# Kernel tuning notes

Hardware: AMD Instinct MI355X
Metric: run time of the kernel (lower is better)

## Reference

```python
import jax, jax.numpy as jnp
import numpy as np
import math

DIM = 1024
H = 16
D = 64
M = 64  # num_features
B = 1
N = 2048


def _orf_omega(key):
    # Orthogonal Random Features: stack Q^T blocks from QR of Gaussian [D,D]
    blocks = []
    n_blocks = (M + D - 1) // D
    for i in range(n_blocks):
        G = jax.random.normal(jax.random.fold_in(key, i), (D, D), dtype=jnp.float32)
        Q, _ = jnp.linalg.qr(G)
        blocks.append(Q.T)
    return jnp.concatenate(blocks, axis=0)[:M]  # [M, D]


def setup_inputs() -> dict:
    key = jax.random.key(0)
    ks = jax.random.split(key, 7)
    inner = H * D
    x = jax.random.normal(ks[0], (B, N, DIM), dtype=jnp.float32)
    omega = _orf_omega(ks[1])
    wq = jax.random.normal(ks[2], (inner, DIM), dtype=jnp.float32) * 0.02
    wk = jax.random.normal(ks[3], (inner, DIM), dtype=jnp.float32) * 0.02
    wv = jax.random.normal(ks[4], (inner, DIM), dtype=jnp.float32) * 0.02
    wo = jax.random.normal(ks[5], (DIM, inner), dtype=jnp.float32) * 0.02
    bo = jnp.zeros((DIM,), dtype=jnp.float32)
    return {"x": x, "omega": omega, "wq": wq, "wk": wk, "wv": wv, "wo": wo, "bo": bo}


def _phi(x, omega):
    # x: [B,H,N,D], omega: [M,D] -> [B,H,N,M]
    proj = jnp.einsum('bhnd,md->bhnm', x, omega)
    norm = 0.5 * jnp.sum(x * x, axis=-1, keepdims=True)
    return jnp.exp(proj - norm) / math.sqrt(M)


def _heads(t):
    b, n, _ = t.shape
    return t.reshape(b, n, H, D).transpose(0, 2, 1, 3)  # [B,H,N,D]


def reference(x, omega, wq, wk, wv, wo, bo):
    b, n, _ = x.shape
    q = _heads(x @ wq.T)
    k = _heads(x @ wk.T)
    v = _heads(x @ wv.T)
    phi_q = _phi(q, omega)  # [B,H,N,M]
    phi_k = _phi(k, omega)
    # causal linear attention: cumulative KV state (naive materialization, faithful to source)
    kv = jnp.einsum('bhnm,bhnd->bhnmd', phi_k, v)       # [B,H,N,M,D]
    kv_cumsum = jnp.cumsum(kv, axis=2)
    k_cumsum = jnp.cumsum(phi_k, axis=2)                # [B,H,N,M]
    out = jnp.einsum('bhnm,bhnmd->bhnd', phi_q, kv_cumsum)
    z = 1.0 / (jnp.einsum('bhnm,bhnm->bhn', phi_q, k_cumsum) + 1e-6)
    out = out * z[..., None]
    out = out.transpose(0, 2, 1, 3).reshape(b, n, H * D)
    return out @ wo.T + bo
```

## Files before the change

kernel.cpp:

```cpp
#include <hip/hip_runtime.h>
#include <hip/hip_bf16.h>

typedef __hip_bfloat16 bf16;
typedef __attribute__((ext_vector_type(8))) short bf16x8;
typedef __attribute__((ext_vector_type(8))) _Float16 f16x8;
typedef __attribute__((ext_vector_type(4))) float f32x4;

constexpr int N_TOK = 2048;
constexpr int DIMM  = 1024;
constexpr int NH    = 16;
constexpr int HD    = 64;
constexpr int FM    = 64;
constexpr int NC    = 32;
constexpr int CS    = 64;

__device__ __forceinline__ float b2f(bf16 v) { return __bfloat162float(v); }
__device__ __forceinline__ unsigned short f2bfu(float v) {
  bf16 h = __float2bfloat16(v);
  return *reinterpret_cast<unsigned short*>(&h);
}
__device__ __forceinline__ unsigned short f2hu(float v) {
  _Float16 h = (_Float16)v;
  return *reinterpret_cast<unsigned short*>(&h);
}

__device__ __forceinline__ void gl_lds16(const void* g, short* l) {
  __builtin_amdgcn_global_load_lds(
      (const __attribute__((address_space(1))) void*)g,
      (__attribute__((address_space(3))) void*)l, 16, 0, 0);
}

__device__ __forceinline__ void split_pack_bf(const float4 v, uint2& ph, uint2& pl) {
  float f[4] = {v.x, v.y, v.z, v.w};
  unsigned short h[4], l[4];
  #pragma unroll
  for (int j = 0; j < 4; j++) {
    bf16 hb = __float2bfloat16(f[j]);
    h[j] = *reinterpret_cast<unsigned short*>(&hb);
    l[j] = f2bfu(f[j] - b2f(hb));
  }
  ph.x = (unsigned)h[0] | ((unsigned)h[1] << 16);
  ph.y = (unsigned)h[2] | ((unsigned)h[3] << 16);
  pl.x = (unsigned)l[0] | ((unsigned)l[1] << 16);
  pl.y = (unsigned)l[2] | ((unsigned)l[3] << 16);
}

__global__ __launch_bounds__(256) void cvt_all(
    const float4* __restrict__ x, const float4* __restrict__ wq,
    const float4* __restrict__ wk, const float4* __restrict__ wv,
    const float4* __restrict__ wo,
    _Float16* __restrict__ x16, _Float16* __restrict__ w16,
    bf16* __restrict__ wo_bf)
{
  int i = blockIdx.x * 256 + threadIdx.x;
  if (i < 524288) {
    float4 v = x[i];
    uint2 p = { (unsigned)f2hu(v.x) | ((unsigned)f2hu(v.y) << 16),
                (unsigned)f2hu(v.z) | ((unsigned)f2hu(v.w) << 16) };
    reinterpret_cast<uint2*>(x16)[i] = p;
  } else if (i < 1310720) {
    int j = i - 524288;
    const float4* src = (j < 262144) ? wq : (j < 524288) ? wk : wv;
    int jj = (j < 262144) ? j : (j < 524288) ? j - 262144 : j - 524288;
    float4 v = src[jj];
    uint2 p = { (unsigned)f2hu(v.x) | ((unsigned)f2hu(v.y) << 16),
                (unsigned)f2hu(v.z) | ((unsigned)f2hu(v.w) << 16) };
    reinterpret_cast<uint2*>(w16)[j] = p;
  } else {
    int j = i - 1310720;
    float4 v = wo[j];
    uint2 p = { (unsigned)f2bfu(v.x) | ((unsigned)f2bfu(v.y) << 16),
                (unsigned)f2bfu(v.z) | ((unsigned)f2bfu(v.w) << 16) };
    reinterpret_cast<uint2*>(wo_bf)[j] = p;
  }
}

__global__ __launch_bounds__(512) void gemm_qkv_f16(
    const _Float16* __restrict__ A16, const _Float16* __restrict__ B16,
    _Float16* __restrict__ Cq, bf16* __restrict__ Cv)
{
  constexpr int K = 1024;
  __shared__ short sA[2][4096], sB[2][4096];
  const int tid = threadIdx.x, lane = tid & 63, wv = tid >> 6;
  const int colBase = blockIdx.x * 128, rowBase = blockIdx.y * 128;
  const int waveRow = (wv >> 2) * 64, waveCol = (wv & 3) * 32;
  const int stR = tid >> 2, stK = (tid & 3) * 8;

  const _Float16* gA = A16 + (size_t)(rowBase + stR) * K + stK;
  const _Float16* gB = B16 + (size_t)(colBase + stR) * K + stK;
  const int ldsOff = wv * 512;

  f32x4 acc[4][2];
  #pragma unroll
  for (int r = 0; r < 4; r++)
    #pragma unroll
    for (int c = 0; c < 2; c++) acc[r][c] = (f32x4){0.f, 0.f, 0.f, 0.f};

  const int frow = lane & 15, fk = (lane >> 4) * 8;
  const int nIter = K / 32;

  gl_lds16(gA, &sA[0][ldsOff]);
  gl_lds16(gB, &sB[0][ldsOff]);

  int buf = 0;
  for (int it = 0; it < nIter; it++) {
    __syncthreads();
    if (it + 1 < nIter) {
      const size_t kb = (size_t)(it + 1) * 32;
      const int nb = buf ^ 1;
      gl_lds16(gA + kb, &sA[nb][ldsOff]);
      gl_lds16(gB + kb, &sB[nb][ldsOff]);
    }
    f16x8 a[4], b[2];
    #pragma unroll
    for (int r = 0; r < 4; r++)
      a[r] = *reinterpret_cast<const f16x8*>(&sA[buf][(waveRow + r * 16 + frow) * 32 + fk]);
    #pragma unroll
    for (int c = 0; c < 2; c++)
      b[c] = *reinterpret_cast<const f16x8*>(&sB[buf][(waveCol + c * 16 + frow) * 32 + fk]);
    #pragma unroll
    for (int r = 0; r < 4; r++)
      #pragma unroll
      for (int c = 0; c < 2; c++)
        acc[r][c] = __builtin_amdgcn_mfma_f32_16x16x32_f16(a[r], b[c], acc[r][c], 0, 0, 0);
    buf ^= 1;
  }

  #pragma unroll
  for (int r = 0; r < 4; r++)
    #pragma unroll
    for (int c = 0; c < 2; c++)
      #pragma unroll
      for (int reg = 0; reg < 4; reg++) {
        int row = rowBase + waveRow + r * 16 + (lane >> 4) * 4 + reg;
        int col = colBase + waveCol + c * 16 + (lane & 15);
        float v = acc[r][c][reg];
        if (col < 2048) Cq[(size_t)row * 2048 + col] = (_Float16)v;
        else            Cv[(size_t)row * 1024 + (col - 2048)] = __float2bfloat16(v);
      }
}

__global__ __launch_bounds__(512) void gemm_bf16_out(
    const bf16* __restrict__ A, const bf16* __restrict__ B,
    const float* __restrict__ bias, float* __restrict__ C)
{
  constexpr int K = 1024;
  __shared__ short sA[2][2048], sB[2][4096];
  const int tid = threadIdx.x, lane = tid & 63, wv = tid >> 6;
  const int rowBase = blockIdx.y * 64, colBase = blockIdx.x * 128;
  const int waveRow = (wv >> 2) * 32, waveCol = (wv & 3) * 32;
  const int stR = tid >> 2, stK = (tid & 3) * 8;
  const bf16* gA = A + (size_t)(rowBase + stR) * K + stK;
  const bf16* gB = B + (size_t)(colBase + stR) * K + stK;
  const int ldsOff = wv * 512;

  f32x4 acc[2][2];
  #pragma unroll
  for (int r = 0; r < 2; r++)
    #pragma unroll
    for (int c = 0; c < 2; c++) acc[r][c] = (f32x4){0.f, 0.f, 0.f, 0.f};

  const int frow = lane & 15, fk = (lane >> 4) * 8;
  const int nIter = K / 32;

  if (wv < 4) gl_lds16(gA, &sA[0][ldsOff]);
  gl_lds16(gB, &sB[0][ldsOff]);

  int buf = 0;
  for (int it = 0; it < nIter; it++) {
    __syncthreads();
    if (it + 1 < nIter) {
      const size_t kb = (size_t)(it + 1) * 32;
      const int nb = buf ^ 1;
      if (wv < 4) gl_lds16(gA + kb, &sA[nb][ldsOff]);
      gl_lds16(gB + kb, &sB[nb][ldsOff]);
    }
    bf16x8 a[2], b[2];
    #pragma unroll
    for (int r = 0; r < 2; r++)
      a[r] = *reinterpret_cast<const bf16x8*>(&sA[buf][(waveRow + r * 16 + frow) * 32 + fk]);
    #pragma unroll
    for (int c = 0; c < 2; c++)
      b[c] = *reinterpret_cast<const bf16x8*>(&sB[buf][(waveCol + c * 16 + frow) * 32 + fk]);
    #pragma unroll
    for (int r = 0; r < 2; r++)
      #pragma unroll
      for (int c = 0; c < 2; c++)
        acc[r][c] = __builtin_amdgcn_mfma_f32_16x16x32_bf16(a[r], b[c], acc[r][c], 0, 0, 0);
    buf ^= 1;
  }

  #pragma unroll
  for (int r = 0; r < 2; r++)
    #pragma unroll
    for (int c = 0; c < 2; c++)
      #pragma unroll
      for (int reg = 0; reg < 4; reg++) {
        int row = rowBase + waveRow + r * 16 + (lane >> 4) * 4 + reg;
        int col = colBase + waveCol + c * 16 + (lane & 15);
        C[(size_t)row * 1024 + col] = acc[r][c][reg] + bias[col];
      }
}

__global__ __launch_bounds__(256) void phi_mfma(
    const _Float16* __restrict__ qk, const float* __restrict__ omega,
    bf16* __restrict__ phiq, bf16* __restrict__ phik)
{
  constexpr int LD = 72;
  __shared__ short sAh[128 * LD], sAl[128 * LD];
  __shared__ short sBh[64 * LD],  sBl[64 * LD];
  __shared__ float sPart[128][2];

  const int tid = threadIdx.x, lane = tid & 63, wv = tid >> 6;
  const int n0 = blockIdx.x * 128, h = blockIdx.y, z = blockIdx.z;
  const int colOff = z * 1024 + h * HD;

  {
    const int r = tid >> 1, half = tid & 1;
    const _Float16* src = qk + (size_t)(n0 + r) * 2048 + colOff + half * 32;
    float ssq = 0.f;
    #pragma unroll
    for (int j8 = 0; j8 < 4; j8++) {
      uint4 raw = reinterpret_cast<const uint4*>(src)[j8];
      const unsigned short* hs = reinterpret_cast<const unsigned short*>(&raw);
      unsigned short hh[8], ll[8];
      #pragma unroll
      for (int j = 0; j < 8; j++) {
        _Float16 hv;
        *reinterpret_cast<unsigned short*>(&hv) = hs[j];
        float f = (float)hv;
        ssq += f * f;
        bf16 hb = __float2bfloat16(f);
        hh[j] = *reinterpret_cast<unsigned short*>(&hb);
        ll[j] = f2bfu(f - b2f(hb));
      }
      int o = r * LD + half * 32 + j8 * 8;
      uint4 ph = { (unsigned)hh[0] | ((unsigned)hh[1] << 16),
                   (unsigned)hh[2] | ((unsigned)hh[3] << 16),
                   (unsigned)hh[4] | ((unsigned)hh[5] << 16),
                   (unsigned)hh[6] | ((unsigned)hh[7] << 16) };
      uint4 pl = { (unsigned)ll[0] | ((unsigned)ll[1] << 16),
                   (unsigned)ll[2] | ((unsigned)ll[3] << 16),
                   (unsigned)ll[4] | ((unsigned)ll[5] << 16),
                   (unsigned)ll[6] | ((unsigned)ll[7] << 16) };
      *reinterpret_cast<uint4*>(&sAh[o]) = ph;
      *reinterpret_cast<uint4*>(&sAl[o]) = pl;
    }
    sPart[r][half] = ssq;
  }
  {
    const int r = tid >> 2, q4 = tid & 3;
    const float* src = omega + (size_t)r * FM + q4 * 16;
    #pragma unroll
    for (int j4 = 0; j4 < 4; j4++) {
      float4 v = reinterpret_cast<const float4*>(src)[j4];
      uint2 ph, pl;
      split_pack_bf(v, ph, pl);
      int o = r * LD + q4 * 16 + j4 * 4;
      *reinterpret_cast<uint2*>(&sBh[o]) = ph;
      *reinterpret_cast<uint2*>(&sBl[o]) = pl;
    }
  }
  __syncthreads();

  const int waveRow = (wv >> 1) * 64, waveCol = (wv & 1) * 32;
  const int frow = lane & 15, fk = (lane >> 4) * 8;

  f32x4 acc[4][2];
  #pragma unroll
  for (int r = 0; r < 4; r++)
    #pragma unroll
    for (int c = 0; c < 2; c++) acc[r][c] = (f32x4){0.f, 0.f, 0.f, 0.f};

  #pragma unroll
  for (int ks = 0; ks < 64; ks += 32) {
    bf16x8 ah[4], al[4], bh[2], bl[2];
    #pragma unroll
    for (int r = 0; r < 4; r++) {
      int o = (waveRow + r * 16 + frow) * LD + ks + fk;
      ah[r] = *reinterpret_cast<const bf16x8*>(&sAh[o]);
      al[r] = *reinterpret_cast<const bf16x8*>(&sAl[o]);
    }
    #pragma unroll
    for (int c = 0; c < 2; c++) {
      int o = (waveCol + c * 16 + frow) * LD + ks + fk;
      bh[c] = *reinterpret_cast<const bf16x8*>(&sBh[o]);
      bl[c] = *reinterpret_cast<const bf16x8*>(&sBl[o]);
    }
    #pragma unroll
    for (int r = 0; r < 4; r++)
      #pragma unroll
      for (int c = 0; c < 2; c++) {
        acc[r][c] = __builtin_amdgcn_mfma_f32_16x16x32_bf16(ah[r], bh[c], acc[r][c], 0, 0, 0);
        acc[r][c] = __builtin_amdgcn_mfma_f32_16x16x32_bf16(ah[r], bl[c], acc[r][c], 0, 0, 0);
        acc[r][c] = __builtin_amdgcn_mfma_f32_16x16x32_bf16(al[r], bh[c], acc[r][c], 0, 0, 0);
      }
  }

  bf16* dst = z ? phik : phiq;
  #pragma unroll
  for (int r = 0; r < 4; r++)
    #pragma unroll
    for (int c = 0; c < 2; c++)
      #pragma unroll
      for (int reg = 0; reg < 4; reg++) {
        int row = waveRow + r * 16 + (lane >> 4) * 4 + reg;
        int col = waveCol + c * 16 + (lane & 15);
        float norm = 0.5f * (sPart[row][0] + sPart[row][1]);
        float v = __expf(fminf(acc[r][c][reg] - norm, 80.f)) * 0.125f;
        dst[((size_t)h * N_TOK + n0 + row) * FM + col] = __float2bfloat16(v);
      }
}

__global__ __launch_bounds__(256) void chunk_sum(
    const bf16* __restrict__ phik, const bf16* __restrict__ vf,
    float* __restrict__ ckv_t, float* __restrict__ ck)
{
  constexpr int LD = 72;
  __shared__ short sVt[64 * LD], sPkt[64 * LD];
  __shared__ float sCp[64][4];
  const int c = blockIdx.x, h = blockIdx.y;
  const int tid = threadIdx.x, lane = tid & 63, wv = tid >> 6;

  {
    int j = tid >> 2, g = tid & 3;
    const bf16* vs = vf + (size_t)(c * CS + j) * DIMM + h * HD + g * 16;
    uint4 v0 = *reinterpret_cast<const uint4*>(vs);
    uint4 v1 = *reinterpret_cast<const uint4*>(vs + 8);
    const unsigned short* pv = (const unsigned short*)&v0;
    #pragma unroll
    for (int e = 0; e < 8; e++) sVt[(g * 16 + e) * LD + j] = (short)pv[e];
    pv = (const unsigned short*)&v1;
    #pragma unroll
    for (int e = 0; e < 8; e++) sVt[(g * 16 + 8 + e) * LD + j] = (short)pv[e];

    const bf16* ks = phik + ((size_t)h * N_TOK + c * CS + j) * FM + g * 16;
    uint4 k0 = *reinterpret_cast<const uint4*>(ks);
    uint4 k1 = *reinterpret_cast<const uint4*>(ks + 8);
    pv = (const unsigned short*)&k0;
    #pragma unroll
    for (int e = 0; e < 8; e++) sPkt[(g * 16 + e) * LD + j] = (short)pv[e];
    pv = (const unsigned short*)&k1;
    #pragma unroll
    for (int e = 0; e < 8; e++) sPkt[(g * 16 + 8 + e) * LD + j] = (short)pv[e];
  }
  __syncthreads();

  const int frow = lane & 15, fk = (lane >> 4) * 8;
  const int rowW = wv * 16;

  f32x4 acc[4];
  #pragma unroll
  for (int mt = 0; mt < 4; mt++) acc[mt] = (f32x4){0.f, 0.f, 0.f, 0.f};
  #pragma unroll
  for (int ks = 0; ks < 64; ks += 32) {
    bf16x8 a = *reinterpret_cast<const bf16x8*>(&sVt[(rowW + frow) * LD + ks + fk]);
    #pragma unroll
    for (int mt = 0; mt < 4; mt++) {
      bf16x8 b = *reinterpret_cast<const bf16x8*>(&sPkt[(mt * 16 + frow) * LD + ks + fk]);
      acc[mt] = __builtin_amdgcn_mfma_f32_16x16x32_bf16(a, b, acc[mt], 0, 0, 0);
    }
  }

  {
    int m = tid >> 2, q = tid & 3;
    float s = 0.f;
    #pragma unroll
    for (int e = 0; e < 16; e++)
      s += b2f(*reinterpret_cast<bf16*>(&sPkt[m * LD + q * 16 + e]));
    sCp[m][q] = s;
  }
  __syncthreads();
  if (tid < 64)
    ck[((size_t)h * NC + c) * FM + tid] = sCp[tid][0] + sCp[tid][1] + sCp[tid][2] + sCp[tid][3];

  float* dst = ckv_t + ((size_t)h * NC + c) * 4096;
  #pragma unroll
  for (int mt = 0; mt < 4; mt++)
    #pragma unroll
    for (int reg = 0; reg < 4; reg++) {
      int gd = rowW + (lane >> 4) * 4 + reg;
      int gm = mt * 16 + (lane & 15);
      dst[gd * 64 + gm] = acc[mt][reg];
    }
}

__global__ __launch_bounds__(256) void prefix_chunks(
    float* __restrict__ ckv, float* __restrict__ ck)
{
  const int h = blockIdx.x, g = blockIdx.y;
  const int cell = g * 256 + threadIdx.x;
  const size_t base = (size_t)h * NC * 4096 + cell;
  float v[NC];
  #pragma unroll
  for (int c = 0; c < NC; c++) v[c] = ckv[base + (size_t)c * 4096];
  float run = 0.f;
  #pragma unroll
  for (int c = 0; c < NC; c++) { float t = v[c]; ckv[base + (size_t)c * 4096] = run; run += t; }
  if (g == 0 && threadIdx.x < 64) {
    const size_t b2 = (size_t)h * NC * FM + threadIdx.x;
    float u[NC];
    #pragma unroll
    for (int c = 0; c < NC; c++) u[c] = ck[b2 + (size_t)c * FM];
    float r2 = 0.f;
    #pragma unroll
    for (int c = 0; c < NC; c++) { float t = u[c]; ck[b2 + (size_t)c * FM] = r2; r2 += t; }
  }
}

__global__ __launch_bounds__(256) void attn_chunk(
    const bf16* __restrict__ phiq, const bf16* __restrict__ phik,
    const bf16* __restrict__ vf, const float* __restrict__ ckv_t,
    const float* __restrict__ ck, bf16* __restrict__ attn_out)
{
  constexpr int LD = 72;
  __shared__ short sPq[64 * LD];
  __shared__ short sPk[64 * LD];
  __shared__ short sAl[64 * LD];
  __shared__ short sVt[64 * LD];
  __shared__ short sSh[64 * LD];
  __shared__ short sSl[64 * LD];
  __shared__ float sKc[64];
  __shared__ float sDp[64][4];
  __shared__ float sDen[64];

  const int c = blockIdx.x, h = blockIdx.y;
  const int tid = threadIdx.x, lane = tid & 63, wv = tid >> 6;

  {
    int r = tid >> 2, g = tid & 3;
    const size_t gb = ((size_t)h * N_TOK + c * CS + r) * FM + g * 16;
    uint4 q0 = *reinterpret_cast<const uint4*>(phiq + gb);
    uint4 q1 = *reinterpret_cast<const uint4*>(phiq + gb + 8);
    uint4 k0 = *reinterpret_cast<const uint4*>(phik + gb);
    uint4 k1 = *reinterpret_cast<const uint4*>(phik + gb + 8);
    int o = r * LD + g * 16;
    *reinterpret_cast<uint4*>(&sPq[o]) = q0; *reinterpret_cast<uint4*>(&sPq[o + 8]) = q1;
    *reinterpret_cast<uint4*>(&sPk[o]) = k0; *reinterpret_cast<uint4*>(&sPk[o + 8]) = k1;
  }
  {
    int j = tid >> 2, g = tid & 3;
    const bf16* vs = vf + (size_t)(c * CS + j) * DIMM + h * HD + g * 16;
    uint4 v0 = *reinterpret_cast<const uint4*>(vs);
    uint4 v1 = *reinterpret_cast<const uint4*>(vs + 8);
    const unsigned short* pv = (const unsigned short*)&v0;
    #pragma unroll
    for (int e = 0; e < 8; e++) sVt[(g * 16 + e) * LD + j] = (short)pv[e];
    pv = (const unsigned short*)&v1;
    #pragma unroll
    for (int e = 0; e < 8; e++) sVt[(g * 16 + 8 + e) * LD + j] = (short)pv[e];
  }
  {
    int d = tid >> 2, mg = tid & 3;
    const float* src = ckv_t + ((size_t)h * NC + c) * 4096 + d * 64 + mg * 16;
    int o = d * LD + mg * 16;
    #pragma unroll
    for (int e4 = 0; e4 < 4; e4++) {
      float4 v = *reinterpret_cast<const float4*>(src + e4 * 4);
      uint2 ph, pl;
      split_pack_bf(v, ph, pl);
      *reinterpret_cast<uint2*>(&sSh[o + e4 * 4]) = ph;
      *reinterpret_cast<uint2*>(&sSl[o + e4 * 4]) = pl;
    }
  }
  if (tid < 64) sKc[tid] = ck[((size_t)h * NC + c) * FM + tid];
  __syncthreads();

  const int frow = lane & 15, fk = (lane >> 4) * 8;
  const int rowW = wv * 16;

  f32x4 accA[4];
  #pragma unroll
  for (int ct = 0; ct < 4; ct++) accA[ct] = (f32x4){0.f, 0.f, 0.f, 0.f};
  #pragma unroll
  for (int ks = 0; ks < 64; ks += 32) {
    bf16x8 a = *reinterpret_cast<const bf16x8*>(&sPq[(rowW + frow) * LD + ks + fk]);
    #pragma unroll
    for (int ct = 0; ct < 4; ct++) {
      bf16x8 b = *reinterpret_cast<const bf16x8*>(&sPk[(ct * 16 + frow) * LD + ks + fk]);
      accA[ct] = __builtin_amdgcn_mfma_f32_16x16x32_bf16(a, b, accA[ct], 0, 0, 0);
    }
  }
  __syncthreads();

  #pragma unroll
  for (int ct = 0; ct < 4; ct++)
    #pragma unroll
    for (int reg = 0; reg < 4; reg++) {
      int gi = rowW + (lane >> 4) * 4 + reg;
      int gj = ct * 16 + (lane & 15);
      float av = (gj <= gi) ? accA[ct][reg] : 0.f;
      bf16 hb = __float2bfloat16(av);
      sPk[gi * LD + gj] = *reinterpret_cast<short*>(&hb);
      unsigned short lu = f2bfu(av - b2f(hb));
      sAl[gi * LD + gj] = (short)lu;
    }
  __syncthreads();

  {
    int i = tid >> 2, q = tid & 3;
    float p = 0.f;
    #pragma unroll
    for (int e = 0; e < 16; e++) {
      int m = q * 16 + e;
      p += b2f(*reinterpret_cast<bf16*>(&sPq[i * LD + m])) * sKc[m];
      p += b2f(*reinterpret_cast<bf16*>(&sPk[i * LD + m]))
         + b2f(*reinterpret_cast<bf16*>(&sAl[i * LD + m]));
    }
    sDp[i][q] = p;
  }

  f32x4 accO[4];
  #pragma unroll
  for (int dt = 0; dt < 4; dt++) accO[dt] = (f32x4){0.f, 0.f, 0.f, 0.f};
  #pragma unroll
  for (int ks = 0; ks < 64; ks += 32) {
    bf16x8 ah = *reinterpret_cast<const bf16x8*>(&sPk[(rowW + frow) * LD + ks + fk]);
    bf16x8 al = *reinterpret_cast<const bf16x8*>(&sAl[(rowW + frow) * LD + ks + fk]);
    bf16x8 aq = *reinterpret_cast<const bf16x8*>(&sPq[(rowW + frow) * LD + ks + fk]);
    #pragma unroll
    for (int dt = 0; dt < 4; dt++) {
      bf16x8 bv = *reinterpret_cast<const bf16x8*>(&sVt[(dt * 16 + frow) * LD + ks + fk]);
      bf16x8 bh = *reinterpret_cast<const bf16x8*>(&sSh[(dt * 16 + frow) * LD + ks + fk]);
      bf16x8 bl = *reinterpret_cast<const bf16x8*>(&sSl[(dt * 16 + frow) * LD + ks + fk]);
      accO[dt] = __builtin_amdgcn_mfma_f32_16x16x32_bf16(ah, bv, accO[dt], 0, 0, 0);
      accO[dt] = __builtin_amdgcn_mfma_f32_16x16x32_bf16(al, bv, accO[dt], 0, 0, 0);
      accO[dt] = __builtin_amdgcn_mfma_f32_16x16x32_bf16(aq, bh, accO[dt], 0, 0, 0);
      accO[dt] = __builtin_amdgcn_mfma_f32_16x16x32_bf16(aq, bl, accO[dt], 0, 0, 0);
    }
  }
  __syncthreads();
  if (tid < 64) {
    float den = sDp[tid][0] + sDp[tid][1] + sDp[tid][2] + sDp[tid][3];
    sDen[tid] = 1.f / (den + 1e-6f);
  }
  __syncthreads();

  #pragma unroll
  for (int dt = 0; dt < 4; dt++)
    #pragma unroll
    for (int reg = 0; reg < 4; reg++) {
      int gi = rowW + (lane >> 4) * 4 + reg;
      int gd = dt * 16 + (lane & 15);
      float v = accO[dt][reg] * sDen[gi];
      attn_out[(size_t)(c * CS + gi) * DIMM + h * HD + gd] = __float2bfloat16(v);
    }
}

extern "C" void kernel_launch(void* const* d_in, const int* in_sizes, int n_in,
                              void* d_out, int out_size, void* d_ws, size_t ws_size,
                              hipStream_t stream) {
  (void)in_sizes; (void)n_in; (void)out_size; (void)ws_size;
  const float* x     = (const float*)d_in[0];
  const float* omega = (const float*)d_in[1];
  const float* wq    = (const float*)d_in[2];
  const float* wk    = (const float*)d_in[3];
  const float* wv    = (const float*)d_in[4];
  const float* wo    = (const float*)d_in[5];
  const float* bo    = (const float*)d_in[6];
  float* out = (float*)d_out;

  char* w = (char*)d_ws;
  _Float16* x16   = (_Float16*)(w);
  _Float16* w16   = (_Float16*)(w + (4u  << 20));
  bf16*     wo_bf = (bf16*)   (w + (10u << 20));
  _Float16* qk    = (_Float16*)(w + (12u << 20));
  bf16*     vbf   = (bf16*)   (w + (20u << 20));
  bf16*     phiq  = (bf16*)   (w + (24u << 20));
  bf16*     phik  = (bf16*)   (w + (28u << 20));
  float*    ckv   = (float*)  (w + (32u << 20));
  float*    ck    = (float*)  (w + (40u << 20));
  bf16*     attnb = (bf16*)x16;

  cvt_all<<<6144, 256, 0, stream>>>((const float4*)x, (const float4*)wq,
                                    (const float4*)wk, (const float4*)wv,
                                    (const float4*)wo,
                                    x16, w16, wo_bf);

  gemm_qkv_f16<<<dim3(24, 16), 512, 0, stream>>>(x16, w16, qk, vbf);

  phi_mfma<<<dim3(N_TOK / 128, NH, 2), 256, 0, stream>>>(qk, omega, phiq, phik);

  chunk_sum<<<dim3(NC, NH), 256, 0, stream>>>(phik, vbf, ckv, ck);
  prefix_chunks<<<dim3(NH, 16), 256, 0, stream>>>(ckv, ck);
  attn_chunk<<<dim3(NC, NH), 256, 0, stream>>>(phiq, phik, vbf, ckv, ck, attnb);

  gemm_bf16_out<<<dim3(8, 32), 512, 0, stream>>>(attnb, wo_bf, bo, out);
}
```

Measured before the change: 143.3 us.

## Fuse phi feature-map computation into QKV GEMM epilogue

The QKV projection GEMM now computes the random-feature map for Q and K directly in its epilogue. Accumulators are split into bf16 hi/lo parts in shared memory, projected onto omega with MFMA, and exponentiated, so the separate phi kernel and the fp16 Q/K intermediate round trip through global memory are gone. This saves one launch and the write and reread of the Q/K buffer. In exchange the GEMM carries a heavier epilogue, a larger shared-memory footprint that may limit occupancy, and extra barriers.

```diff
diff --git a/kernel.cpp b/kernel.cpp
--- a/kernel.cpp
+++ b/kernel.cpp
@@ -75,12 +75,16 @@
   }
 }
 
-__global__ __launch_bounds__(512) void gemm_qkv_f16(
+__global__ __launch_bounds__(512, 4) void gemm_qkv_phi(
     const _Float16* __restrict__ A16, const _Float16* __restrict__ B16,
-    _Float16* __restrict__ Cq, bf16* __restrict__ Cv)
+    const float* __restrict__ omega,
+    bf16* __restrict__ phiq, bf16* __restrict__ phik, bf16* __restrict__ Cv)
 {
   constexpr int K = 1024;
-  __shared__ short sA[2][4096], sB[2][4096];
+  __shared__ alignas(16) char smemRaw[56320];
+  short* sA = (short*)smemRaw;
+  short* sB = sA + 8192;
+
   const int tid = threadIdx.x, lane = tid & 63, wv = tid >> 6;
   const int colBase = blockIdx.x * 128, rowBase = blockIdx.y * 128;
   const int waveRow = (wv >> 2) * 64, waveCol = (wv & 3) * 32;
@@ -96,11 +100,11 @@
     #pragma unroll
     for (int c = 0; c < 2; c++) acc[r][c] = (f32x4){0.f, 0.f, 0.f, 0.f};
 
-  const int frow = lane & 15, fk = (lane >> 4) * 8;
+  const int frow = lane & 15, fk = (lane >> 4) * 8, quad = lane >> 4;
   const int nIter = K / 32;
 
-  gl_lds16(gA, &sA[0][ldsOff]);
-  gl_lds16(gB, &sB[0][ldsOff]);
+  gl_lds16(gA, &sA[ldsOff]);
+  gl_lds16(gB, &sB[ldsOff]);
 
   int buf = 0;
   for (int it = 0; it < nIter; it++) {
@@ -108,16 +112,16 @@
     if (it + 1 < nIter) {
       const size_t kb = (size_t)(it + 1) * 32;
       const int nb = buf ^ 1;
-      gl_lds16(gA + kb, &sA[nb][ldsOff]);
-      gl_lds16(gB + kb, &sB[nb][ldsOff]);
+      gl_lds16(gA + kb, &sA[nb * 4096 + ldsOff]);
+      gl_lds16(gB + kb, &sB[nb * 4096 + ldsOff]);
     }
     f16x8 a[4], b[2];
     #pragma unroll
     for (int r = 0; r < 4; r++)
-      a[r] = *reinterpret_cast<const f16x8*>(&sA[buf][(waveRow + r * 16 + frow) * 32 + fk]);
+      a[r] = *reinterpret_cast<const f16x8*>(&sA[buf * 4096 + (waveRow + r * 16 + frow) * 32 + fk]);
     #pragma unroll
     for (int c = 0; c < 2; c++)
-      b[c] = *reinterpret_cast<const f16x8*>(&sB[buf][(waveCol + c * 16 + frow) * 32 + fk]);
+      b[c] = *reinterpret_cast<const f16x8*>(&sB[buf * 4096 + (waveCol + c * 16 + frow) * 32 + fk]);
     #pragma unroll
     for (int r = 0; r < 4; r++)
       #pragma unroll
@@ -125,19 +129,111 @@
         acc[r][c] = __builtin_amdgcn_mfma_f32_16x16x32_f16(a[r], b[c], acc[r][c], 0, 0, 0);
     buf ^= 1;
   }
+  __syncthreads();
+
+  if (colBase >= 2048) {
+    #pragma unroll
+    for (int r = 0; r < 4; r++)
+      #pragma unroll
+      for (int c = 0; c < 2; c++)
+        #pragma unroll
+        for (int reg = 0; reg < 4; reg++) {
+          int row = rowBase + waveRow + r * 16 + quad * 4 + reg;
+          int col = colBase - 2048 + waveCol + c * 16 + (lane & 15);
+          Cv[(size_t)row * 1024 + col] = __float2bfloat16(acc[r][c][reg]);
+        }
+    return;
+  }
+
+  constexpr int LD = 72;
+  short* sQh = (short*)smemRaw;
+  short* sQl = sQh + 9216;
+  short* sOh = sQl + 9216;
+  short* sOl = sOh + 4608;
+  float* sNorm = (float*)(sOl + 4608);
+
+  const bool isQ = (colBase < 1024);
+  const int hPairBase = (isQ ? colBase : (colBase - 1024)) >> 6;
+  bf16* dstBase = isQ ? phiq : phik;
+  const int headSel = (wv & 3) >> 1;
+
+  {
+    int r = tid >> 3, cg = (tid & 7) * 8;
+    const float* src = omega + r * 64 + cg;
+    float4 v0 = *reinterpret_cast<const float4*>(src);
+    float4 v1 = *reinterpret_cast<const float4*>(src + 4);
+    uint2 ph, pl;
+    split_pack_bf(v0, ph, pl);
+    *reinterpret_cast<uint2*>(&sOh[r * LD + cg])     = ph;
+    *reinterpret_cast<uint2*>(&sOl[r * LD + cg])     = pl;
+    split_pack_bf(v1, ph, pl);
+    *reinterpret_cast<uint2*>(&sOh[r * LD + cg + 4]) = ph;
+    *reinterpret_cast<uint2*>(&sOl[r * LD + cg + 4]) = pl;
+  }
+  if (tid < 256) sNorm[tid] = 0.f;
+  __syncthreads();
 
   #pragma unroll
   for (int r = 0; r < 4; r++)
     #pragma unroll
-    for (int c = 0; c < 2; c++)
+    for (int reg = 0; reg < 4; reg++) {
+      float s = acc[r][0][reg] * acc[r][0][reg] + acc[r][1][reg] * acc[r][1][reg];
+      s += __shfl_xor(s, 1); s += __shfl_xor(s, 2);
+      s += __shfl_xor(s, 4); s += __shfl_xor(s, 8);
+      if ((lane & 15) == 0) {
+        int row = waveRow + r * 16 + quad * 4 + reg;
+        atomicAdd(&sNorm[headSel * 128 + row], s);
+      }
+    }
+
+  #pragma unroll
+  for (int hh = 0; hh < 2; hh++) {
+    if (headSel == hh) {
+      #pragma unroll
+      for (int r = 0; r < 4; r++)
+        #pragma unroll
+        for (int c = 0; c < 2; c++)
+          #pragma unroll
+          for (int reg = 0; reg < 4; reg++) {
+            int row = waveRow + r * 16 + quad * 4 + reg;
+            int lc = (waveCol & 63) + c * 16 + (lane & 15);
+            float v = acc[r][c][reg];
+            bf16 hb = __float2bfloat16(v);
+            sQh[row * LD + lc] = *reinterpret_cast<short*>(&hb);
+            sQl[row * LD + lc] = (short)f2bfu(v - b2f(hb));
+          }
+    }
+    __syncthreads();
+
+    f32x4 acc2[4];
+    #pragma unroll
+    for (int ct = 0; ct < 4; ct++) acc2[ct] = (f32x4){0.f, 0.f, 0.f, 0.f};
+    #pragma unroll
+    for (int ks = 0; ks < 64; ks += 32) {
+      bf16x8 ah = *reinterpret_cast<const bf16x8*>(&sQh[(wv * 16 + frow) * LD + ks + fk]);
+      bf16x8 al = *reinterpret_cast<const bf16x8*>(&sQl[(wv * 16 + frow) * LD + ks + fk]);
+      #pragma unroll
+      for (int ct = 0; ct < 4; ct++) {
+        bf16x8 bh = *reinterpret_cast<const bf16x8*>(&sOh[(ct * 16 + frow) * LD + ks + fk]);
+        bf16x8 bl = *reinterpret_cast<const bf16x8*>(&sOl[(ct * 16 + frow) * LD + ks + fk]);
+        acc2[ct] = __builtin_amdgcn_mfma_f32_16x16x32_bf16(ah, bh, acc2[ct], 0, 0, 0);
+        acc2[ct] = __builtin_amdgcn_mfma_f32_16x16x32_bf16(ah, bl, acc2[ct], 0, 0, 0);
+        acc2[ct] = __builtin_amdgcn_mfma_f32_16x16x32_bf16(al, bh, acc2[ct], 0, 0, 0);
+      }
+    }
+    const int h = hPairBase + hh;
+    #pragma unroll
+    for (int ct = 0; ct < 4; ct++)
       #pragma unroll
       for (int reg = 0; reg < 4; reg++) {
-        int row = rowBase + waveRow + r * 16 + (lane >> 4) * 4 + reg;
-        int col = colBase + waveCol + c * 16 + (lane & 15);
-        float v = acc[r][c][reg];
-        if (col < 2048) Cq[(size_t)row * 2048 + col] = (_Float16)v;
-        else            Cv[(size_t)row * 1024 + (col - 2048)] = __float2bfloat16(v);
+        int row = wv * 16 + quad * 4 + reg;
+        int m = ct * 16 + (lane & 15);
+        float norm = 0.5f * sNorm[hh * 128 + row];
+        float v = __expf(fminf(acc2[ct][reg] - norm, 80.f)) * 0.125f;
+        dstBase[((size_t)h * N_TOK + rowBase + row) * FM + m] = __float2bfloat16(v);
       }
+    __syncthreads();
+  }
 }
 
 __global__ __launch_bounds__(512) void gemm_bf16_out(
@@ -199,116 +295,6 @@
         int row = rowBase + waveRow + r * 16 + (lane >> 4) * 4 + reg;
         int col = colBase + waveCol + c * 16 + (lane & 15);
         C[(size_t)row * 1024 + col] = acc[r][c][reg] + bias[col];
-      }
-}
-
-__global__ __launch_bounds__(256) void phi_mfma(
-    const _Float16* __restrict__ qk, const float* __restrict__ omega,
-    bf16* __restrict__ phiq, bf16* __restrict__ phik)
-{
-  constexpr int LD = 72;
-  __shared__ short sAh[128 * LD], sAl[128 * LD];
-  __shared__ short sBh[64 * LD],  sBl[64 * LD];
-  __shared__ float sPart[128][2];
-
-  const int tid = threadIdx.x, lane = tid & 63, wv = tid >> 6;
-  const int n0 = blockIdx.x * 128, h = blockIdx.y, z = blockIdx.z;
-  const int colOff = z * 1024 + h * HD;
-
-  {
-    const int r = tid >> 1, half = tid & 1;
-    const _Float16* src = qk + (size_t)(n0 + r) * 2048 + colOff + half * 32;
-    float ssq = 0.f;
-    #pragma unroll
-    for (int j8 = 0; j8 < 4; j8++) {
-      uint4 raw = reinterpret_cast<const uint4*>(src)[j8];
-      const unsigned short* hs = reinterpret_cast<const unsigned short*>(&raw);
-      unsigned short hh[8], ll[8];
-      #pragma unroll
-      for (int j = 0; j < 8; j++) {
-        _Float16 hv;
-        *reinterpret_cast<unsigned short*>(&hv) = hs[j];
-        float f = (float)hv;
-        ssq += f * f;
-        bf16 hb = __float2bfloat16(f);
-        hh[j] = *reinterpret_cast<unsigned short*>(&hb);
-        ll[j] = f2bfu(f - b2f(hb));
-      }
-      int o = r * LD + half * 32 + j8 * 8;
-      uint4 ph = { (unsigned)hh[0] | ((unsigned)hh[1] << 16),
-                   (unsigned)hh[2] | ((unsigned)hh[3] << 16),
-                   (unsigned)hh[4] | ((unsigned)hh[5] << 16),
-                   (unsigned)hh[6] | ((unsigned)hh[7] << 16) };
-      uint4 pl = { (unsigned)ll[0] | ((unsigned)ll[1] << 16),
-                   (unsigned)ll[2] | ((unsigned)ll[3] << 16),
-                   (unsigned)ll[4] | ((unsigned)ll[5] << 16),
-                   (unsigned)ll[6] | ((unsigned)ll[7] << 16) };
-      *reinterpret_cast<uint4*>(&sAh[o]) = ph;
-      *reinterpret_cast<uint4*>(&sAl[o]) = pl;
-    }
-    sPart[r][half] = ssq;
-  }
-  {
-    const int r = tid >> 2, q4 = tid & 3;
-    const float* src = omega + (size_t)r * FM + q4 * 16;
-    #pragma unroll
-    for (int j4 = 0; j4 < 4; j4++) {
-      float4 v = reinterpret_cast<const float4*>(src)[j4];
-      uint2 ph, pl;
-      split_pack_bf(v, ph, pl);
-      int o = r * LD + q4 * 16 + j4 * 4;
-      *reinterpret_cast<uint2*>(&sBh[o]) = ph;
-      *reinterpret_cast<uint2*>(&sBl[o]) = pl;
-    }
-  }
-  __syncthreads();
-
-  const int waveRow = (wv >> 1) * 64, waveCol = (wv & 1) * 32;
-  const int frow = lane & 15, fk = (lane >> 4) * 8;
-
-  f32x4 acc[4][2];
-  #pragma unroll
-  for (int r = 0; r < 4; r++)
-    #pragma unroll
-    for (int c = 0; c < 2; c++) acc[r][c] = (f32x4){0.f, 0.f, 0.f, 0.f};
-
-  #pragma unroll
-  for (int ks = 0; ks < 64; ks += 32) {
-    bf16x8 ah[4], al[4], bh[2], bl[2];
-    #pragma unroll
-    for (int r = 0; r < 4; r++) {
-      int o = (waveRow + r * 16 + frow) * LD + ks + fk;
-      ah[r] = *reinterpret_cast<const bf16x8*>(&sAh[o]);
-      al[r] = *reinterpret_cast<const bf16x8*>(&sAl[o]);
-    }
-    #pragma unroll
-    for (int c = 0; c < 2; c++) {
-      int o = (waveCol + c * 16 + frow) * LD + ks + fk;
-      bh[c] = *reinterpret_cast<const bf16x8*>(&sBh[o]);
-      bl[c] = *reinterpret_cast<const bf16x8*>(&sBl[o]);
-    }
-    #pragma unroll
-    for (int r = 0; r < 4; r++)
-      #pragma unroll
-      for (int c = 0; c < 2; c++) {
-        acc[r][c] = __builtin_amdgcn_mfma_f32_16x16x32_bf16(ah[r], bh[c], acc[r][c], 0, 0, 0);
-        acc[r][c] = __builtin_amdgcn_mfma_f32_16x16x32_bf16(ah[r], bl[c], acc[r][c], 0, 0, 0);
-        acc[r][c] = __builtin_amdgcn_mfma_f32_16x16x32_bf16(al[r], bh[c], acc[r][c], 0, 0, 0);
-      }
-  }
-
-  bf16* dst = z ? phik : phiq;
-  #pragma unroll
-  for (int r = 0; r < 4; r++)
-    #pragma unroll
-    for (int c = 0; c < 2; c++)
-      #pragma unroll
-      for (int reg = 0; reg < 4; reg++) {
-        int row = waveRow + r * 16 + (lane >> 4) * 4 + reg;
-        int col = waveCol + c * 16 + (lane & 15);
-        float norm = 0.5f * (sPart[row][0] + sPart[row][1]);
-        float v = __expf(fminf(acc[r][c][reg] - norm, 80.f)) * 0.125f;
-        dst[((size_t)h * N_TOK + n0 + row) * FM + col] = __float2bfloat16(v);
       }
 }
 
@@ -564,12 +550,11 @@
   _Float16* x16   = (_Float16*)(w);
   _Float16* w16   = (_Float16*)(w + (4u  << 20));
   bf16*     wo_bf = (bf16*)   (w + (10u << 20));
-  _Float16* qk    = (_Float16*)(w + (12u << 20));
-  bf16*     vbf   = (bf16*)   (w + (20u << 20));
-  bf16*     phiq  = (bf16*)   (w + (24u << 20));
-  bf16*     phik  = (bf16*)   (w + (28u << 20));
-  float*    ckv   = (float*)  (w + (32u << 20));
-  float*    ck    = (float*)  (w + (40u << 20));
+  bf16*     vbf   = (bf16*)   (w + (12u << 20));
+  bf16*     phiq  = (bf16*)   (w + (16u << 20));
+  bf16*     phik  = (bf16*)   (w + (20u << 20));
+  float*    ckv   = (float*)  (w + (24u << 20));
+  float*    ck    = (float*)  (w + (32u << 20));
   bf16*     attnb = (bf16*)x16;
 
   cvt_all<<<6144, 256, 0, stream>>>((const float4*)x, (const float4*)wq,
@@ -577,9 +562,7 @@
                                     (const float4*)wo,
                                     x16, w16, wo_bf);
 
-  gemm_qkv_f16<<<dim3(24, 16), 512, 0, stream>>>(x16, w16, qk, vbf);
-
-  phi_mfma<<<dim3(N_TOK / 128, NH, 2), 256, 0, stream>>>(qk, omega, phiq, phik);
+  gemm_qkv_phi<<<dim3(24, 16), 512, 0, stream>>>(x16, w16, omega, phiq, phik, vbf);
 
   chunk_sum<<<dim3(NC, NH), 256, 0, stream>>>(phik, vbf, ckv, ck);
   prefix_chunks<<<dim3(NH, 16), 256, 0, stream>>>(ckv, ck);
```

Measured after the change: 142.6 us. No clear change (-0.5%).
